# Kernel tuning notes

Measured on AMD Instinct MI355X. Metric: run time of the kernel, lower is better.

Reference implementation:

```python
import jax, jax.numpy as jnp
import numpy as np

DIM = 192
T, H, W = 6, 8, 8
NH = 6
HD = DIM // NH
HW = H * W
N = T * HW
SCALE = HD ** (-0.5)
B_ = 128


def _sine_pos_enc():
    # Faithful port of get_sine_position_encoding(window_size[1:], dim // 2).
    npf = DIM // 2
    ones = jnp.ones((1, H, W), jnp.float32)
    y_embed = jnp.cumsum(ones, axis=1)
    x_embed = jnp.cumsum(ones, axis=2)
    two_pi = 2.0 * np.pi
    y_embed = y_embed / (y_embed[:, -1:, :] + 1e-6) * two_pi
    x_embed = x_embed / (x_embed[:, :, -1:] + 1e-6) * two_pi
    dim_t = jnp.arange(npf, dtype=jnp.float32)
    dim_t = 10000.0 ** (2.0 * jnp.floor(dim_t / 2.0) / npf)
    pos_x = x_embed[:, :, :, None] / dim_t
    pos_y = y_embed[:, :, :, None] / dim_t
    pos_x = jnp.stack((jnp.sin(pos_x[..., 0::2]), jnp.cos(pos_x[..., 1::2])), axis=4).reshape(1, H, W, npf)
    pos_y = jnp.stack((jnp.sin(pos_y[..., 0::2]), jnp.cos(pos_y[..., 1::2])), axis=4).reshape(1, H, W, npf)
    pos = jnp.concatenate((pos_y, pos_x), axis=3)  # (1, H, W, DIM)
    return pos.reshape(1, HW, DIM)


def setup_inputs() -> dict:
    key = jax.random.key(0)
    ks = jax.random.split(key, 6)
    s = 0.02
    return {
        "x": jax.random.normal(ks[0], (B_, N, DIM), jnp.float32),
        "Wqkv": jax.random.normal(ks[1], (3 * DIM, DIM), jnp.float32) * s,
        "Wproj": jax.random.normal(ks[2], (DIM, 2 * DIM), jnp.float32) * s,
        "bproj": jnp.zeros((DIM,), jnp.float32),
        "gamma": jnp.ones((DIM,), jnp.float32),
        "beta": jnp.zeros((DIM,), jnp.float32),
        "W1": jax.random.normal(ks[3], (DIM, DIM), jnp.float32) * s,
        "b1": jnp.zeros((DIM,), jnp.float32),
        "W2": jax.random.normal(ks[4], (DIM, DIM), jnp.float32) * s,
        "b2": jnp.zeros((DIM,), jnp.float32),
    }


def reference(x, Wqkv, Wproj, bproj, gamma, beta, W1, b1, W2, b2):
    b = x.shape[0]
    pos = jnp.tile(_sine_pos_enc(), (1, T, 1))  # (1, N, DIM)
    qkv = (x + pos) @ Wqkv.T                      # (b, N, 3*DIM)
    qkv = qkv.reshape(b, N, 3, NH, HD).transpose(2, 0, 3, 1, 4)
    # temporal chunks: (b, NH, T, HW, HD)
    q = qkv[0].reshape(b, NH, T, HW, HD)
    k = qkv[1].reshape(b, NH, T, HW, HD)
    v = qkv[2].reshape(b, NH, T, HW, HD)
    # all T x T cross-frame attention pairs at once
    scores = jnp.einsum('bhind,bhjmd->ijbhnm', q * SCALE, k)  # (T,T,b,NH,HW,HW)
    attn = jax.nn.softmax(scores, axis=-1)
    o = jnp.einsum('ijbhnm,bhjmd->ijbnhd', attn, v).reshape(T, T, b, HW, DIM)
    # Faithful to torch's x.view(-1, B_, HW, C): raw reinterpretation, not a transpose.
    x_tmp = x.reshape(T, b, HW, DIM)
    xi = jnp.broadcast_to(x_tmp[:, None], (T, T, b, HW, DIM))
    x_att = jnp.concatenate((o, xi), axis=-1)     # (T,T,b,HW,2*DIM)
    y = x_att @ Wproj.T + bproj
    mu = jnp.mean(y, axis=-1, keepdims=True)
    var = jnp.var(y, axis=-1, keepdims=True)
    y = (y - mu) / jnp.sqrt(var + 1e-5) * gamma + beta
    y = jax.nn.gelu(y @ W1.T + b1, approximate=False) @ W2.T + b2
    acc = jnp.sum(y, axis=1)                       # sum over j -> (T,b,HW,DIM)
    x_out = x + acc.transpose(1, 0, 2, 3).reshape(b, N, DIM) / T
    return jnp.concatenate((x, x_out), axis=-1)
```

## Files before the change

### kernel.cpp

```cpp
#include <hip/hip_runtime.h>
#include <cmath>

#define TT   6
#define NB   128
#define DIM  192
#define SCALE 0.17677669529663687f

typedef __attribute__((ext_vector_type(8))) short v8s;
typedef __attribute__((ext_vector_type(4))) float v4f;

__device__ __forceinline__ short f2bf(float f) {
  union { float f; unsigned u; } v; v.f = f;
  unsigned r = v.u + 0x7fffu + ((v.u >> 16) & 1u);
  return (short)(r >> 16);
}

__global__ void prep_kernel(const float* __restrict__ Wqkv, const float* __restrict__ Wproj,
                            const float* __restrict__ W1, const float* __restrict__ W2,
                            short* __restrict__ dWqkv, short* __restrict__ dWproj,
                            short* __restrict__ dW1, short* __restrict__ dW2,
                            float* __restrict__ pos) {
  int idx = blockIdx.x * 256 + threadIdx.x;
  const float* src = nullptr; short* dst = nullptr; int off = 0;
  if (idx < 27648)      { src = Wqkv;  dst = dWqkv;  off = idx; }
  else if (idx < 46080) { src = Wproj; dst = dWproj; off = idx - 27648; }
  else if (idx < 55296) { src = W1;    dst = dW1;    off = idx - 46080; }
  else if (idx < 64512) { src = W2;    dst = dW2;    off = idx - 55296; }
  else if (idx < 67584) {
    int p0 = (idx - 64512) * 4;
    float4 r;
    float* rp = (float*)&r;
#pragma unroll
    for (int jj = 0; jj < 4; jj++) {
      int p = p0 + jj;
      int row = p / 192, c = p - row * 192;
      int e  = (c < 96) ? (row >> 3) : (row & 7);
      int cc = (c < 96) ? c : c - 96;
      int m = cc >> 1;
      float embed = (float)(e + 1) * (6.283185307179586f / 8.000001f);
      float dt = powf(10000.0f, (float)m * (1.0f / 48.0f));
      float ang = embed / dt;
      rp[jj] = (cc & 1) ? cosf(ang) : sinf(ang);
    }
    *(float4*)(pos + p0) = r;
    return;
  } else return;
  const float* s = src + off * 4;
  short4 r;
  r.x = f2bf(s[0]); r.y = f2bf(s[1]); r.z = f2bf(s[2]); r.w = f2bf(s[3]);
  *(short4*)(dst + off * 4) = r;
}

__global__ __launch_bounds__(256) void qkv_kernel(
    const float* __restrict__ x, const float* __restrict__ pos,
    const short* __restrict__ Wqkv_bf,
    short* __restrict__ Qb, short* __restrict__ Kb, short* __restrict__ Vtb) {
  __shared__ short XP[64 * 200];
  int bid = blockIdx.x;
  int t = bid % TT, b = bid / TT;
  int tid = threadIdx.x, w = tid >> 6, lane = tid & 63;
  int l15 = lane & 15, quad = lane >> 4;
  const float* xrow = x + (size_t)(b * (TT * 64) + t * 64) * DIM;
  for (int c = tid; c < 64 * 24; c += 256) {
    int row = c / 24, col8 = (c - (c / 24) * 24) * 8;
    const float* xs = xrow + row * DIM + col8;
    const float* pp = pos + row * DIM + col8;
    v8s r8;
#pragma unroll
    for (int jj = 0; jj < 8; jj++) r8[jj] = f2bf(xs[jj] + pp[jj]);
    *(v8s*)(XP + row * 200 + col8) = r8;
  }
  __syncthreads();
  const v4f vzero = {0.f, 0.f, 0.f, 0.f};
  size_t obase = (size_t)(b * TT + t) * 64 * DIM;
#pragma unroll
  for (int cti = 0; cti < 9; cti++) {
    int r0 = w * 144 + cti * 16;
    v4f acc[4] = {vzero, vzero, vzero, vzero};
#pragma unroll
    for (int ks = 0; ks < 6; ks++) {
      v8s a = *(const v8s*)(Wqkv_bf + (size_t)(r0 + l15) * 192 + ks * 32 + quad * 8);
#pragma unroll
      for (int nt = 0; nt < 4; nt++) {
        v8s bb = *(const v8s*)(XP + (nt * 16 + l15) * 200 + ks * 32 + quad * 8);
        acc[nt] = __builtin_amdgcn_mfma_f32_16x16x32_bf16(a, bb, acc[nt], 0, 0, 0);
      }
    }
    int R = r0 + quad * 4;
#pragma unroll
    for (int nt = 0; nt < 4; nt++) {
      int hw = nt * 16 + l15;
      if (R < 192) {
        short4 s;
        s.x = f2bf(acc[nt][0] * SCALE); s.y = f2bf(acc[nt][1] * SCALE);
        s.z = f2bf(acc[nt][2] * SCALE); s.w = f2bf(acc[nt][3] * SCALE);
        *(short4*)(Qb + obase + (size_t)hw * 192 + R) = s;
      } else if (R < 384) {
        short4 s;
        s.x = f2bf(acc[nt][0]); s.y = f2bf(acc[nt][1]);
        s.z = f2bf(acc[nt][2]); s.w = f2bf(acc[nt][3]);
        *(short4*)(Kb + obase + (size_t)hw * 192 + (R - 192)) = s;
      } else {
#pragma unroll
        for (int r = 0; r < 4; r++)
          Vtb[obase + (size_t)(R - 384 + r) * 64 + hw] = f2bf(acc[nt][r]);
      }
    }
  }
}

__global__ __launch_bounds__(512, 6) void fused_all(
    const float* __restrict__ x,
    const short* __restrict__ Qb, const short* __restrict__ Kb,
    const short* __restrict__ Vtb,
    const short* __restrict__ Wproj_bf, const short* __restrict__ W1_bf,
    const short* __restrict__ W2_bf,
    const float* __restrict__ bproj, const float* __restrict__ gamma,
    const float* __restrict__ beta, const float* __restrict__ b1,
    const float* __restrict__ b2,
    float* __restrict__ out) {
  __shared__ short SP[64 * 200];
  __shared__ short XI[64 * 200];
  __shared__ float LNp[64][4][2];

  int bid = blockIdx.x;
  int xcd = bid & 7, idx6 = bid >> 3;
  int bq = idx6 / TT;
  int b = xcd * 16 + bq, i = idx6 - bq * TT;

  int tid = threadIdx.x, w = tid >> 6, lane = tid & 63;
  int l15 = lane & 15, quad = lane >> 4;
  int wc = w & 3, wh = w >> 2;
  int cb = wc * 48;
  const v4f vzero = {0.f, 0.f, 0.f, 0.f};

  const float* xi = x + (size_t)(i * NB + b) * 64 * DIM;
  for (int c = tid; c < 64 * 24; c += 512) {
    int row = c / 24, col8 = (c - (c / 24) * 24) * 8;
    const float* xs = xi + row * DIM + col8;
    v8s r8;
#pragma unroll
    for (int jj = 0; jj < 8; jj++) r8[jj] = f2bf(xs[jj]);
    *(v8s*)(XI + row * 200 + col8) = r8;
  }

  const short* Qi = Qb + (size_t)(b * TT + i) * 64 * DIM;
  v8s qa[3];
#pragma unroll
  for (int hh = 0; hh < 3; hh++)
    qa[hh] = *(const v8s*)(Qi + (size_t)(wc * 16 + l15) * 192 + (wh * 3 + hh) * 32 + quad * 8);

  v4f acc[3][2];
#pragma unroll
  for (int cti = 0; cti < 3; cti++)
#pragma unroll
    for (int nt = 0; nt < 2; nt++) acc[cti][nt] = vzero;

  __syncthreads();

  int srcA = l15 + ((lane & 16) << 1);
  int srcB = srcA + 16;
  bool hiq = (lane & 32) != 0;

  for (int j = 0; j < TT; j++) {
    __syncthreads();
    const short* Kj = Kb + (size_t)(b * TT + j) * 64 * DIM;
    const short* Vj = Vtb + (size_t)(b * TT + j) * 64 * DIM;

#pragma unroll
    for (int hh = 0; hh < 3; hh++) {
      int h = wh * 3 + hh;
      v4f S[4];
#pragma unroll
      for (int cta = 0; cta < 4; cta++) {
        v8s akq = *(const v8s*)(Kj + (size_t)(cta * 16 + l15) * 192 + h * 32 + quad * 8);
        S[cta] = __builtin_amdgcn_mfma_f32_16x16x32_bf16(akq, qa[hh], vzero, 0, 0, 0);
      }
      float mx = -1e30f;
#pragma unroll
      for (int cta = 0; cta < 4; cta++)
#pragma unroll
        for (int r = 0; r < 4; r++) mx = fmaxf(mx, S[cta][r]);
      mx = fmaxf(mx, __shfl_xor(mx, 16, 64));
      mx = fmaxf(mx, __shfl_xor(mx, 32, 64));
      float sum = 0.f;
#pragma unroll
      for (int cta = 0; cta < 4; cta++)
#pragma unroll
        for (int r = 0; r < 4; r++) {
          float e = __expf(S[cta][r] - mx);
          S[cta][r] = e; sum += e;
        }
      sum += __shfl_xor(sum, 16, 64);
      sum += __shfl_xor(sum, 32, 64);
      float inv = 1.0f / sum;
      unsigned pk[4][2];
#pragma unroll
      for (int cta = 0; cta < 4; cta++) {
        float a0 = S[cta][0] * inv, a1 = S[cta][1] * inv;
        float a2 = S[cta][2] * inv, a3 = S[cta][3] * inv;
        __asm__("v_cvt_pk_bf16_f32 %0, %1, %2" : "=v"(pk[cta][0]) : "v"(a0), "v"(a1));
        __asm__("v_cvt_pk_bf16_f32 %0, %1, %2" : "=v"(pk[cta][1]) : "v"(a2), "v"(a3));
      }
      unsigned t00 = (unsigned)__shfl((int)pk[0][0], srcA), t10 = (unsigned)__shfl((int)pk[1][0], srcA);
      unsigned t01 = (unsigned)__shfl((int)pk[0][1], srcA), t11 = (unsigned)__shfl((int)pk[1][1], srcA);
      unsigned u00 = (unsigned)__shfl((int)pk[0][0], srcB), u10 = (unsigned)__shfl((int)pk[1][0], srcB);
      unsigned u01 = (unsigned)__shfl((int)pk[0][1], srcB), u11 = (unsigned)__shfl((int)pk[1][1], srcB);
      unsigned s20 = (unsigned)__shfl((int)pk[2][0], srcA), s30 = (unsigned)__shfl((int)pk[3][0], srcA);
      unsigned s21 = (unsigned)__shfl((int)pk[2][1], srcA), s31 = (unsigned)__shfl((int)pk[3][1], srcA);
      unsigned v20 = (unsigned)__shfl((int)pk[2][0], srcB), v30 = (unsigned)__shfl((int)pk[3][0], srcB);
      unsigned v21 = (unsigned)__shfl((int)pk[2][1], srcB), v31 = (unsigned)__shfl((int)pk[3][1], srcB);
      union { unsigned u[4]; v8s v; } B0, B1;
      B0.u[0] = hiq ? t10 : t00;  B0.u[1] = hiq ? t11 : t01;
      B0.u[2] = hiq ? u10 : u00;  B0.u[3] = hiq ? u11 : u01;
      B1.u[0] = hiq ? s30 : s20;  B1.u[1] = hiq ? s31 : s21;
      B1.u[2] = hiq ? v30 : v20;  B1.u[3] = hiq ? v31 : v21;
#pragma unroll
      for (int ct2 = 0; ct2 < 2; ct2++) {
        v8s av0 = *(const v8s*)(Vj + (size_t)(h * 32 + ct2 * 16 + l15) * 64 + quad * 8);
        v8s av1 = *(const v8s*)(Vj + (size_t)(h * 32 + ct2 * 16 + l15) * 64 + 32 + quad * 8);
        v4f o = __builtin_amdgcn_mfma_f32_16x16x32_bf16(av0, B0.v, vzero, 0, 0, 0);
        o = __builtin_amdgcn_mfma_f32_16x16x32_bf16(av1, B1.v, o, 0, 0, 0);
        short4 s;
        s.x = f2bf(o[0]); s.y = f2bf(o[1]); s.z = f2bf(o[2]); s.w = f2bf(o[3]);
        *(short4*)(&SP[(wc * 16 + l15) * 200 + h * 32 + ct2 * 16 + quad * 4]) = s;
      }
    }
    __syncthreads();

    v4f y1[3][2];
#pragma unroll
    for (int cti = 0; cti < 3; cti++)
#pragma unroll
      for (int nt = 0; nt < 2; nt++) y1[cti][nt] = vzero;
#pragma unroll
    for (int ks = 0; ks < 6; ks++) {
      v8s bo[2];
#pragma unroll
      for (int nt = 0; nt < 2; nt++)
        bo[nt] = *(const v8s*)(SP + (wh * 32 + nt * 16 + l15) * 200 + ks * 32 + quad * 8);
#pragma unroll
      for (int cti = 0; cti < 3; cti++) {
        v8s a = *(const v8s*)(Wproj_bf + (size_t)(cb + cti * 16 + l15) * 384 + ks * 32 + quad * 8);
#pragma unroll
        for (int nt = 0; nt < 2; nt++)
          y1[cti][nt] = __builtin_amdgcn_mfma_f32_16x16x32_bf16(a, bo[nt], y1[cti][nt], 0, 0, 0);
      }
    }
#pragma unroll
    for (int ks = 0; ks < 6; ks++) {
      v8s bxi[2];
#pragma unroll
      for (int nt = 0; nt < 2; nt++)
        bxi[nt] = *(const v8s*)(XI + (wh * 32 + nt * 16 + l15) * 200 + ks * 32 + quad * 8);
#pragma unroll
      for (int cti = 0; cti < 3; cti++) {
        v8s a = *(const v8s*)(Wproj_bf + (size_t)(cb + cti * 16 + l15) * 384 + 192 + ks * 32 + quad * 8);
#pragma unroll
        for (int nt = 0; nt < 2; nt++)
          y1[cti][nt] = __builtin_amdgcn_mfma_f32_16x16x32_bf16(a, bxi[nt], y1[cti][nt], 0, 0, 0);
      }
    }
#pragma unroll
    for (int cti = 0; cti < 3; cti++) {
      float4 bp4 = *(const float4*)(bproj + cb + cti * 16 + quad * 4);
#pragma unroll
      for (int nt = 0; nt < 2; nt++) {
        y1[cti][nt][0] += bp4.x; y1[cti][nt][1] += bp4.y;
        y1[cti][nt][2] += bp4.z; y1[cti][nt][3] += bp4.w;
      }
    }
#pragma unroll
    for (int nt = 0; nt < 2; nt++) {
      float s1 = 0.f, s2 = 0.f;
#pragma unroll
      for (int cti = 0; cti < 3; cti++)
#pragma unroll
        for (int r = 0; r < 4; r++) { float v = y1[cti][nt][r]; s1 += v; s2 += v * v; }
      s1 += __shfl_xor(s1, 16, 64); s2 += __shfl_xor(s2, 16, 64);
      s1 += __shfl_xor(s1, 32, 64); s2 += __shfl_xor(s2, 32, 64);
      if (quad == 0) {
        LNp[wh * 32 + nt * 16 + l15][wc][0] = s1;
        LNp[wh * 32 + nt * 16 + l15][wc][1] = s2;
      }
    }
    __syncthreads();
    float mu[2], rs[2];
#pragma unroll
    for (int nt = 0; nt < 2; nt++) {
      int row = wh * 32 + nt * 16 + l15;
      float s1 = 0.f, s2 = 0.f;
#pragma unroll
      for (int ww = 0; ww < 4; ww++) { s1 += LNp[row][ww][0]; s2 += LNp[row][ww][1]; }
      float m = s1 * (1.0f / 192.0f);
      mu[nt] = m; rs[nt] = rsqrtf(s2 * (1.0f / 192.0f) - m * m + 1e-5f);
    }
#pragma unroll
    for (int cti = 0; cti < 3; cti++) {
      float4 g4 = *(const float4*)(gamma + cb + cti * 16 + quad * 4);
      float4 be4 = *(const float4*)(beta + cb + cti * 16 + quad * 4);
#pragma unroll
      for (int nt = 0; nt < 2; nt++) {
        short4 s;
        s.x = f2bf((y1[cti][nt][0] - mu[nt]) * rs[nt] * g4.x + be4.x);
        s.y = f2bf((y1[cti][nt][1] - mu[nt]) * rs[nt] * g4.y + be4.y);
        s.z = f2bf((y1[cti][nt][2] - mu[nt]) * rs[nt] * g4.z + be4.z);
        s.w = f2bf((y1[cti][nt][3] - mu[nt]) * rs[nt] * g4.w + be4.w);
        *(short4*)(&SP[(wh * 32 + nt * 16 + l15) * 200 + cb + cti * 16 + quad * 4]) = s;
      }
    }
    __syncthreads();

    v4f y2[3][2];
#pragma unroll
    for (int cti = 0; cti < 3; cti++)
#pragma unroll
      for (int nt = 0; nt < 2; nt++) y2[cti][nt] = vzero;
#pragma unroll
    for (int ks = 0; ks < 6; ks++) {
      v8s bh[2];
#pragma unroll
      for (int nt = 0; nt < 2; nt++)
        bh[nt] = *(const v8s*)(SP + (wh * 32 + nt * 16 + l15) * 200 + ks * 32 + quad * 8);
#pragma unroll
      for (int cti = 0; cti < 3; cti++) {
        v8s a = *(const v8s*)(W1_bf + (size_t)(cb + cti * 16 + l15) * 192 + ks * 32 + quad * 8);
#pragma unroll
        for (int nt = 0; nt < 2; nt++)
          y2[cti][nt] = __builtin_amdgcn_mfma_f32_16x16x32_bf16(a, bh[nt], y2[cti][nt], 0, 0, 0);
      }
    }
    __syncthreads();
#pragma unroll
    for (int cti = 0; cti < 3; cti++) {
      float4 b14 = *(const float4*)(b1 + cb + cti * 16 + quad * 4);
#pragma unroll
      for (int nt = 0; nt < 2; nt++) {
        float vv[4] = {y2[cti][nt][0] + b14.x, y2[cti][nt][1] + b14.y,
                       y2[cti][nt][2] + b14.z, y2[cti][nt][3] + b14.w};
        short sv[4];
#pragma unroll
        for (int r = 0; r < 4; r++) {
          float v = vv[r];
          float t = 0.79788456080286536f * (v + 0.044715f * v * v * v);
          float e = __expf(2.0f * t);
          float th = 1.0f - 2.0f / (e + 1.0f);
          sv[r] = f2bf(0.5f * v * (1.0f + th));
        }
        short4 s;
        s.x = sv[0]; s.y = sv[1]; s.z = sv[2]; s.w = sv[3];
        *(short4*)(&SP[(wh * 32 + nt * 16 + l15) * 200 + cb + cti * 16 + quad * 4]) = s;
      }
    }
    __syncthreads();

#pragma unroll
    for (int ks = 0; ks < 6; ks++) {
      v8s bh[2];
#pragma unroll
      for (int nt = 0; nt < 2; nt++)
        bh[nt] = *(const v8s*)(SP + (wh * 32 + nt * 16 + l15) * 200 + ks * 32 + quad * 8);
#pragma unroll
      for (int cti = 0; cti < 3; cti++) {
        v8s a = *(const v8s*)(W2_bf + (size_t)(cb + cti * 16 + l15) * 192 + ks * 32 + quad * 8);
#pragma unroll
        for (int nt = 0; nt < 2; nt++)
          acc[cti][nt] = __builtin_amdgcn_mfma_f32_16x16x32_bf16(a, bh[nt], acc[cti][nt], 0, 0, 0);
      }
    }
  }

#pragma unroll
  for (int cti = 0; cti < 3; cti++) {
    int cc0 = cb + cti * 16 + quad * 4;
    float4 b24 = *(const float4*)(b2 + cc0);
#pragma unroll
    for (int nt = 0; nt < 2; nt++) {
      int hw = wh * 32 + nt * 16 + l15;
      size_t nrow = (size_t)b * 384 + (size_t)i * 64 + hw;
      float4 xv = *(const float4*)(x + nrow * DIM + cc0);
      float4 o4;
      o4.x = xv.x + acc[cti][nt][0] * (1.0f / 6.0f) + b24.x;
      o4.y = xv.y + acc[cti][nt][1] * (1.0f / 6.0f) + b24.y;
      o4.z = xv.z + acc[cti][nt][2] * (1.0f / 6.0f) + b24.z;
      o4.w = xv.w + acc[cti][nt][3] * (1.0f / 6.0f) + b24.w;
      *(float4*)(out + nrow * 384 + 192 + cc0) = o4;
    }
  }
  for (int c = tid; c < 64 * 48; c += 512) {
    int row = c / 48, col4 = (c - (c / 48) * 48) * 4;
    size_t nrow = (size_t)b * 384 + (size_t)i * 64 + row;
    *(float4*)(out + nrow * 384 + col4) = *(const float4*)(x + nrow * DIM + col4);
  }
}

extern "C" void kernel_launch(void* const* d_in, const int* in_sizes, int n_in,
                              void* d_out, int out_size, void* d_ws, size_t ws_size,
                              hipStream_t stream) {
  (void)in_sizes; (void)n_in; (void)out_size; (void)ws_size;
  const float* x     = (const float*)d_in[0];
  const float* Wqkv  = (const float*)d_in[1];
  const float* Wproj = (const float*)d_in[2];
  const float* bproj = (const float*)d_in[3];
  const float* gamma = (const float*)d_in[4];
  const float* beta  = (const float*)d_in[5];
  const float* W1    = (const float*)d_in[6];
  const float* b1    = (const float*)d_in[7];
  const float* W2    = (const float*)d_in[8];
  const float* b2    = (const float*)d_in[9];
  float* out = (float*)d_out;

  short* Wqkv_bf  = (short*)d_ws;
  short* Wproj_bf = Wqkv_bf + 110592;
  short* W1_bf    = Wproj_bf + 73728;
  short* W2_bf    = W1_bf + 36864;
  float* pos_f    = (float*)(W2_bf + 36864);
  short* Qb       = (short*)(pos_f + 12288);
  short* Kb       = Qb + 9437184;
  short* Vtb      = Kb + 9437184;

  prep_kernel<<<dim3(264), dim3(256), 0, stream>>>(
      Wqkv, Wproj, W1, W2, Wqkv_bf, Wproj_bf, W1_bf, W2_bf, pos_f);
  qkv_kernel<<<dim3(TT * NB), dim3(256), 0, stream>>>(x, pos_f, Wqkv_bf, Qb, Kb, Vtb);
  fused_all<<<dim3(TT * NB), dim3(512), 0, stream>>>(
      x, Qb, Kb, Vtb, Wproj_bf, W1_bf, W2_bf, bproj, gamma, beta, b1, b2, out);
}
```

Baseline: 637.4 us.

## Remap QKV blocks across XCDs and stage final output through LDS for coalesced stores

The QKV kernel's block index is remapped so that consecutive blocks on the same XCD handle the same batch group, which should improve L2 locality on the multi-die GPU. The final epilogue now writes the scaled MFMA accumulators to shared memory in two half-tile passes. All threads then read them back row-wise, so the x load, the residual add and both output halves are written with contiguous float4 accesses. This removes the scattered per-lane stores of the accumulator layout and reuses a single x load for both outputs. The cost is extra LDS traffic and barriers.

```diff
diff --git a/kernel.cpp b/kernel.cpp
--- a/kernel.cpp
+++ b/kernel.cpp
@@ -57,7 +57,9 @@
     short* __restrict__ Qb, short* __restrict__ Kb, short* __restrict__ Vtb) {
   __shared__ short XP[64 * 200];
   int bid = blockIdx.x;
-  int t = bid % TT, b = bid / TT;
+  int xcd = bid & 7, idx = bid >> 3;
+  int bq = idx / TT;
+  int b = xcd * 16 + bq, t = idx - bq * TT;
   int tid = threadIdx.x, w = tid >> 6, lane = tid & 63;
   int l15 = lane & 15, quad = lane >> 4;
   const float* xrow = x + (size_t)(b * (TT * 64) + t * 64) * DIM;
@@ -370,27 +372,39 @@
     }
   }
 
-#pragma unroll
-  for (int cti = 0; cti < 3; cti++) {
-    int cc0 = cb + cti * 16 + quad * 4;
-    float4 b24 = *(const float4*)(b2 + cc0);
-#pragma unroll
-    for (int nt = 0; nt < 2; nt++) {
-      int hw = wh * 32 + nt * 16 + l15;
-      size_t nrow = (size_t)b * 384 + (size_t)i * 64 + hw;
-      float4 xv = *(const float4*)(x + nrow * DIM + cc0);
+  float* SPf = (float*)SP;
+#pragma unroll
+  for (int pass = 0; pass < 2; pass++) {
+    __syncthreads();
+    if (wh == pass) {
+#pragma unroll
+      for (int cti = 0; cti < 3; cti++)
+#pragma unroll
+        for (int nt = 0; nt < 2; nt++) {
+          float4 o4;
+          o4.x = acc[cti][nt][0] * (1.0f / 6.0f);
+          o4.y = acc[cti][nt][1] * (1.0f / 6.0f);
+          o4.z = acc[cti][nt][2] * (1.0f / 6.0f);
+          o4.w = acc[cti][nt][3] * (1.0f / 6.0f);
+          *(float4*)(&SPf[(nt * 16 + l15) * 196 + cb + cti * 16 + quad * 4]) = o4;
+        }
+    }
+    __syncthreads();
+    for (int c = tid; c < 1536; c += 512) {
+      int r32 = c / 48, col4 = (c - r32 * 48) * 4;
+      int row = pass * 32 + r32;
+      size_t nrow = (size_t)b * 384 + (size_t)i * 64 + row;
+      float4 xv = *(const float4*)(x + nrow * DIM + col4);
+      float4 b24 = *(const float4*)(b2 + col4);
+      float4 av = *(const float4*)(&SPf[r32 * 196 + col4]);
       float4 o4;
-      o4.x = xv.x + acc[cti][nt][0] * (1.0f / 6.0f) + b24.x;
-      o4.y = xv.y + acc[cti][nt][1] * (1.0f / 6.0f) + b24.y;
-      o4.z = xv.z + acc[cti][nt][2] * (1.0f / 6.0f) + b24.z;
-      o4.w = xv.w + acc[cti][nt][3] * (1.0f / 6.0f) + b24.w;
-      *(float4*)(out + nrow * 384 + 192 + cc0) = o4;
-    }
-  }
-  for (int c = tid; c < 64 * 48; c += 512) {
-    int row = c / 48, col4 = (c - (c / 48) * 48) * 4;
-    size_t nrow = (size_t)b * 384 + (size_t)i * 64 + row;
-    *(float4*)(out + nrow * 384 + col4) = *(const float4*)(x + nrow * DIM + col4);
+      o4.x = xv.x + av.x + b24.x;
+      o4.y = xv.y + av.y + b24.y;
+      o4.z = xv.z + av.z + b24.z;
+      o4.w = xv.w + av.w + b24.w;
+      *(float4*)(out + nrow * 384 + col4) = xv;
+      *(float4*)(out + nrow * 384 + 192 + col4) = o4;
+    }
   }
 }
 
```

Result: no change. 632.6 us (-0.8%).
